# Optimization experiments

Hardware: AMD Instinct MI355X
Metric: run time of the kernel (lower is better)

The kernel has to match this reference:

```python
import jax, jax.numpy as jnp
import numpy as np

N_NODES = 100000
N_EDGES = 1600000
D = 128


def setup_inputs() -> dict:
    key = jax.random.key(0)
    ks = jax.random.split(key, 10)
    s = 1.0 / np.sqrt(D)
    return {
        "feat": jax.random.normal(ks[0], (N_NODES, D), dtype=jnp.float32),
        "W_self0": jax.random.normal(ks[1], (D, D), dtype=jnp.float32) * s,
        "W_neigh0": jax.random.normal(ks[2], (D, D), dtype=jnp.float32) * s,
        "b0": jnp.zeros((D,), dtype=jnp.float32),
        "W_self1": jax.random.normal(ks[3], (D, D), dtype=jnp.float32) * s,
        "W_neigh1": jax.random.normal(ks[4], (D, D), dtype=jnp.float32) * s,
        "b1": jnp.zeros((D,), dtype=jnp.float32),
        "ln_g": jnp.ones((D,), dtype=jnp.float32),
        "ln_b": jnp.zeros((D,), dtype=jnp.float32),
        "edge_src": jax.random.randint(ks[5], (N_EDGES,), 0, N_NODES, dtype=jnp.int32),
        "edge_dst": jax.random.randint(ks[6], (N_EDGES,), 0, N_NODES, dtype=jnp.int32),
        "in_deg": jax.random.randint(ks[7], (N_NODES,), 1, 64, dtype=jnp.int32),
    }


def _sage_layer(h, src, dst, inv_deg, W_self, W_neigh, b):
    # mean aggregation over incoming neighbors: gather -> segment_sum -> scale
    msg = jax.ops.segment_sum(h[src], dst, num_segments=N_NODES)  # [N, d]
    h_neigh = msg * inv_deg[:, None]
    return h @ W_self + h_neigh @ W_neigh + b


def _layer_norm(x, g, b, eps=1e-5):
    mu = jnp.mean(x, axis=-1, keepdims=True)
    var = jnp.mean((x - mu) ** 2, axis=-1, keepdims=True)
    return (x - mu) * jax.lax.rsqrt(var + eps) * g + b


def reference(feat, W_self0, W_neigh0, b0, W_self1, W_neigh1, b1, ln_g, ln_b,
              edge_src, edge_dst, in_deg):
    # Eval mode: dropout = identity, no EmbeddingSelector / reg loss.
    inv_deg = 1.0 / jnp.maximum(in_deg, 1).astype(feat.dtype)
    h = _sage_layer(feat, edge_src, edge_dst, inv_deg, W_self0, W_neigh0, b0)
    h = _layer_norm(h, ln_g, ln_b)
    h = jax.nn.relu(h)
    h = _sage_layer(h, edge_src, edge_dst, inv_deg, W_self1, W_neigh1, b1)
    return h
```

## Files before the change

kernel.cpp:

```cpp
#include <hip/hip_runtime.h>

#define D 128
#define NN 100000
#define PB 391
#define EPB 4096
#define PREP_BLKS 12756

typedef __attribute__((ext_vector_type(8))) short short8;
typedef __attribute__((ext_vector_type(16))) float floatx16;
typedef __attribute__((ext_vector_type(2))) float floatx2;

__device__ inline unsigned short bf16_rne(float f) {
    unsigned int u = __float_as_uint(f);
    u += 0x7fff + ((u >> 16) & 1);
    return (unsigned short)(u >> 16);
}
__device__ inline unsigned char fp8_enc1(float f) {
    return (unsigned char)(__builtin_amdgcn_cvt_pk_fp8_f32(f, f, 0, false) & 0xff);
}


__global__ __launch_bounds__(256) void prep_count_kernel(
    const float* __restrict__ feat, unsigned short* __restrict__ feat16,
    unsigned char* __restrict__ feat8,
    const float* __restrict__ Ws0, const float* __restrict__ Wn0,
    const float* __restrict__ Ws1, const float* __restrict__ Wn1,
    unsigned short* __restrict__ wt0, unsigned short* __restrict__ wt1,
    const int* __restrict__ dst, unsigned int* __restrict__ bucketCnt,
    unsigned int* __restrict__ blockBase, int E)
{
    __shared__ unsigned int h[PB];
    int bid = blockIdx.x;
    if (bid < 12500) {
        int i = bid * 256 + threadIdx.x;
        float4 v = *(const float4*)(feat + (size_t)i * 4);
        unsigned short u[4] = { bf16_rne(v.x), bf16_rne(v.y), bf16_rne(v.z), bf16_rne(v.w) };
        int n  = i >> 5;
        int d0 = (i & 31) * 4;
        size_t f = (size_t)(n >> 5) * 4096 + (size_t)((d0 >> 3) * 32 + (n & 31)) * 8 + (d0 & 7);
        *(uint2*)(feat16 + f) = *(uint2*)u;
        int w = __builtin_amdgcn_cvt_pk_fp8_f32(v.x, v.y, 0, false);
        w = __builtin_amdgcn_cvt_pk_fp8_f32(v.z, v.w, w, true);
        ((unsigned int*)feat8)[i] = (unsigned int)w;
    } else if (bid < PREP_BLKS) {
        int i = (bid - 12500) * 256 + threadIdx.x;
        int layer = i >> 15;
        int r = i & 32767;
        int n = r >> 8;
        int k = r & 255;
        const float* Ws = layer ? Ws1 : Ws0;
        const float* Wn = layer ? Wn1 : Wn0;
        float v = (k < 128) ? Ws[(size_t)k * 128 + n] : Wn[(size_t)(k - 128) * 128 + n];
        unsigned short* wt = layer ? wt1 : wt0;
        int ct = n >> 5, nn = n & 31;
        int hs = k >> 7, k7 = k & 127;
        int kc = k7 >> 4, hf = (k7 >> 3) & 1, j = k7 & 7;
        int frag = ((((ct * 2 + hs) * 8 + kc) * 2 + hf) * 32 + nn) * 8 + j;
        wt[frag] = bf16_rne(v);
    } else {
        const int b = bid - PREP_BLKS;
        const int t = threadIdx.x;
        for (int i = t; i < PB; i += 256) h[i] = 0;
        __syncthreads();
        const int base = b * EPB;
#pragma unroll
        for (int k = 0; k < EPB / 256; k++) {
            int e = base + k * 256 + t;
            if (e < E) atomicAdd(&h[(unsigned)dst[e] >> 8], 1u);
        }
        __syncthreads();
        for (int i = t; i < PB; i += 256) {
            unsigned int c = h[i];
            unsigned int o = 0;
            if (c) o = atomicAdd(&bucketCnt[i], c);
            blockBase[(size_t)b * PB + i] = o;
        }
    }
}

__global__ __launch_bounds__(512) void part_scan_kernel(
    const unsigned int* __restrict__ bucketCnt, unsigned int* __restrict__ bucketStart,
    int E)
{
    __shared__ unsigned int sd[512];
    int t = threadIdx.x;
    unsigned int v = (t < PB) ? bucketCnt[t] : 0u;
    sd[t] = v; __syncthreads();
    for (int off = 1; off < 512; off <<= 1) {
        unsigned int x = (t >= off) ? sd[t - off] : 0u;
        __syncthreads();
        sd[t] += x;
        __syncthreads();
    }
    if (t < PB) bucketStart[t] = sd[t] - v;
    if (t == 0) bucketStart[PB] = (unsigned int)E;
}

__global__ __launch_bounds__(256) void part_scatter_kernel(
    const int* __restrict__ src, const int* __restrict__ dst,
    const unsigned int* __restrict__ bucketStart,
    const unsigned int* __restrict__ blockBase,
    unsigned int* __restrict__ pairs, int E)
{
    __shared__ unsigned int h[PB];
    const int t = threadIdx.x;
    const int b = blockIdx.x;
    for (int i = t; i < PB; i += 256) h[i] = 0;
    __syncthreads();
    const int base = b * EPB;
#pragma unroll
    for (int k = 0; k < EPB / 256; k++) {
        int e = base + k * 256 + t;
        if (e < E) {
            unsigned int d = (unsigned int)dst[e];
            unsigned int bk = d >> 8;
            unsigned int lr = atomicAdd(&h[bk], 1u);
            unsigned int pos = bucketStart[bk] + blockBase[(size_t)b * PB + bk] + lr;
            pairs[pos] = ((unsigned int)src[e] << 8) | (d & 255u);
        }
    }
}

__global__ __launch_bounds__(256) void part_fine_kernel(
    const unsigned int* __restrict__ pairs, const unsigned int* __restrict__ bucketStart,
    int* __restrict__ row_ptr, int* __restrict__ col, int N, int E)
{
    __shared__ unsigned int h[256], sc[256], pos[256];
    const int t = threadIdx.x;
    const int b = blockIdx.x;
    h[t] = 0;
    __syncthreads();
    const unsigned int ebeg = bucketStart[b];
    const unsigned int eend = bucketStart[b + 1];
    for (unsigned int i = ebeg + t; i < eend; i += 256)
        atomicAdd(&h[pairs[i] & 255u], 1u);
    __syncthreads();
    sc[t] = h[t]; __syncthreads();
    for (int off = 1; off < 256; off <<= 1) {
        unsigned int x = (t >= off) ? sc[t - off] : 0u;
        __syncthreads();
        sc[t] += x;
        __syncthreads();
    }
    unsigned int excl = sc[t] - h[t];
    int node = b * 256 + t;
    if (node < N) row_ptr[node] = (int)(ebeg + excl);
    pos[t] = ebeg + excl;
    if (b == 0 && t == 0) row_ptr[N] = E;
    __syncthreads();
    for (unsigned int i = ebeg + t; i < eend; i += 256) {
        unsigned int p = pairs[i];
        unsigned int w = atomicAdd(&pos[p & 255u], 1u);
        col[w] = (int)(p >> 8);
    }
}

__global__ __launch_bounds__(256) void gather8_kernel(
    const unsigned char* __restrict__ h8, const int* __restrict__ row_ptr,
    const int* __restrict__ col, const int* __restrict__ in_deg,
    unsigned short* __restrict__ msg16, int N)
{
    const int wave = threadIdx.x >> 6;
    const int lane = threadIdx.x & 63;
    const int quad = lane >> 4;
    const int ln16 = lane & 15;
    const int node = (blockIdx.x * 4 + wave) * 4 + quad;
    if (node >= N) return;

    const size_t lo = (size_t)ln16 * 8;
    int beg = row_ptr[node];
    int end = row_ptr[node + 1];

    float f[8] = {0.f,0.f,0.f,0.f,0.f,0.f,0.f,0.f};
    int j = beg;
    for (; j + 4 <= end; j += 4) {
        int c0 = col[j], c1 = col[j + 1], c2 = col[j + 2], c3 = col[j + 3];
        uint2 u0 = *(const uint2*)(h8 + (size_t)c0 * D + lo);
        uint2 u1 = *(const uint2*)(h8 + (size_t)c1 * D + lo);
        uint2 u2 = *(const uint2*)(h8 + (size_t)c2 * D + lo);
        uint2 u3 = *(const uint2*)(h8 + (size_t)c3 * D + lo);
#pragma unroll
        for (int q = 0; q < 4; q++) {
            uint2 u = q == 0 ? u0 : q == 1 ? u1 : q == 2 ? u2 : u3;
            floatx2 p0 = __builtin_amdgcn_cvt_pk_f32_fp8((int)u.x, false);
            floatx2 p1 = __builtin_amdgcn_cvt_pk_f32_fp8((int)u.x, true);
            floatx2 p2 = __builtin_amdgcn_cvt_pk_f32_fp8((int)u.y, false);
            floatx2 p3 = __builtin_amdgcn_cvt_pk_f32_fp8((int)u.y, true);
            f[0] += p0.x; f[1] += p0.y; f[2] += p1.x; f[3] += p1.y;
            f[4] += p2.x; f[5] += p2.y; f[6] += p3.x; f[7] += p3.y;
        }
    }
    for (; j < end; ++j) {
        uint2 u = *(const uint2*)(h8 + (size_t)col[j] * D + lo);
        floatx2 p0 = __builtin_amdgcn_cvt_pk_f32_fp8((int)u.x, false);
        floatx2 p1 = __builtin_amdgcn_cvt_pk_f32_fp8((int)u.x, true);
        floatx2 p2 = __builtin_amdgcn_cvt_pk_f32_fp8((int)u.y, false);
        floatx2 p3 = __builtin_amdgcn_cvt_pk_f32_fp8((int)u.y, true);
        f[0] += p0.x; f[1] += p0.y; f[2] += p1.x; f[3] += p1.y;
        f[4] += p2.x; f[5] += p2.y; f[6] += p3.x; f[7] += p3.y;
    }
    int dg = in_deg[node];
    float invd = 1.f / (float)(dg > 1 ? dg : 1);
    unsigned short us[8];
#pragma unroll
    for (int i = 0; i < 8; i++) us[i] = bf16_rne(f[i] * invd);
    size_t fo = (size_t)(node >> 5) * 4096 + ((size_t)ln16 * 32 + (node & 31)) * 8;
    *(uint4*)(msg16 + fo) = *(const uint4*)us;
}

__global__ __launch_bounds__(256, 3) void mfma32_kernel(
    const unsigned short* __restrict__ A16, const unsigned short* __restrict__ Msg16,
    const unsigned short* __restrict__ Wt,
    const float* __restrict__ bias,
    const float* __restrict__ ln_g, const float* __restrict__ ln_b,
    unsigned short* __restrict__ Out16, unsigned char* __restrict__ Out8,
    float* __restrict__ Out32, int N, int do_ln)
{
    __shared__ char smem[49152];

    const int tid  = threadIdx.x;
    const int wave = tid >> 6;
    const int lane = tid & 63;
    const int half = lane >> 5;
    const int n32  = lane & 31;
    const int brow0 = blockIdx.x * 128;
    const int wrow0 = brow0 + wave * 32;

    const int NT = N >> 5;
    int tile = wrow0 >> 5;
    if (tile >= NT) tile = NT - 1;
    const short8* Af = (const short8*)(A16   + (size_t)tile * 4096);
    const short8* Mf = (const short8*)(Msg16 + (size_t)tile * 4096);

    floatx16 acc[4];
#pragma unroll
    for (int ct = 0; ct < 4; ct++)
#pragma unroll
        for (int r = 0; r < 16; r++) acc[ct][r] = 0.f;

#pragma unroll
    for (int hs = 0; hs < 2; hs++) {
        const short8* Sf = hs ? Mf : Af;
#pragma unroll
        for (int kc = 0; kc < 8; kc++) {
            short8 a = Sf[kc * 64 + lane];
#pragma unroll
            for (int ct = 0; ct < 4; ct++) {
                short8 b = *(const short8*)(Wt + ((size_t)((ct * 2 + hs) * 8 + kc) * 64 + lane) * 8);
                acc[ct] = __builtin_amdgcn_mfma_f32_32x32x16_bf16(a, b, acc[ct], 0, 0, 0);
            }
        }
    }

    float bb[4];
#pragma unroll
    for (int ct = 0; ct < 4; ct++) bb[ct] = bias[ct * 32 + n32];

    float v[4][16];
#pragma unroll
    for (int ct = 0; ct < 4; ct++)
#pragma unroll
        for (int r = 0; r < 16; r++) v[ct][r] = acc[ct][r] + bb[ct];

    if (do_ln) {
        float gg[4], be[4];
#pragma unroll
        for (int ct = 0; ct < 4; ct++) {
            gg[ct] = ln_g[ct * 32 + n32];
            be[ct] = ln_b[ct * 32 + n32];
        }
        float s[16], s2[16];
#pragma unroll
        for (int r = 0; r < 16; r++) {
            s[r]  = v[0][r] + v[1][r] + v[2][r] + v[3][r];
            s2[r] = v[0][r]*v[0][r] + v[1][r]*v[1][r] + v[2][r]*v[2][r] + v[3][r]*v[3][r];
        }
#pragma unroll
        for (int off = 1; off < 32; off <<= 1) {
#pragma unroll
            for (int r = 0; r < 16; r++) {
                s[r]  += __shfl_xor(s[r],  off);
                s2[r] += __shfl_xor(s2[r], off);
            }
        }
        unsigned char* sO8 = (unsigned char*)smem + 32768;
#pragma unroll
        for (int r = 0; r < 16; r++) {
            float mean = s[r] * (1.f / 128.f);
            float var  = s2[r] * (1.f / 128.f) - mean * mean;
            float rstd = rsqrtf(var + 1e-5f);
            int brow = wave * 32 + (r & 3) + 8 * (r >> 2) + 4 * half;
#pragma unroll
            for (int ct = 0; ct < 4; ct++) {
                float t = (v[ct][r] - mean) * rstd * gg[ct] + be[ct];
                t = t > 0.f ? t : 0.f;
                int slot = (ct * 4 + (n32 >> 3)) ^ (brow & 15);
                *(unsigned short*)(smem + brow * 256 + slot * 16 + (n32 & 7) * 2) = bf16_rne(t);
                sO8[brow * 128 + ct * 32 + n32] = fp8_enc1(t);
            }
        }
        __syncthreads();
#pragma unroll
        for (int i = 0; i < 8; i++) {
            int ch = tid + i * 256;
            int tl = ch >> 9, p = ch & 511, kc2 = p >> 5, rr = p & 31;
            if (brow0 + tl * 32 + rr < N)
                *(uint4*)(Out16 + (size_t)brow0 * D + ch * 8) =
                    *(const uint4*)&smem[(tl * 32 + rr) * 256 + ((kc2 ^ (rr & 15)) * 16)];
        }
#pragma unroll
        for (int i = 0; i < 4; i++) {
            int ch = tid + i * 256;
            if (brow0 + (ch >> 3) < N)
                *(uint4*)(Out8 + (size_t)brow0 * D + ch * 16) = *(const uint4*)&sO8[ch * 16];
        }
    } else {
#pragma unroll
        for (int r = 0; r < 16; r++) {
            int row = wrow0 + (r & 3) + 8 * (r >> 2) + 4 * half;
            if (row < N) {
#pragma unroll
                for (int ct = 0; ct < 4; ct++)
                    Out32[(size_t)row * D + ct * 32 + n32] = v[ct][r];
            }
        }
    }
}

extern "C" void kernel_launch(void* const* d_in, const int* in_sizes, int n_in,
                              void* d_out, int out_size, void* d_ws, size_t ws_size,
                              hipStream_t stream)
{
    const float* feat = (const float*)d_in[0];
    const float* Ws0  = (const float*)d_in[1];
    const float* Wn0  = (const float*)d_in[2];
    const float* b0   = (const float*)d_in[3];
    const float* Ws1  = (const float*)d_in[4];
    const float* Wn1  = (const float*)d_in[5];
    const float* b1   = (const float*)d_in[6];
    const float* lng  = (const float*)d_in[7];
    const float* lnb  = (const float*)d_in[8];
    const int* esrc   = (const int*)d_in[9];
    const int* edst   = (const int*)d_in[10];
    const int* indeg  = (const int*)d_in[11];

    const int N = NN;
    const int E = in_sizes[9];

    float* out = (float*)d_out;

    const int nblk = (E + EPB - 1) / EPB;
    char* ws = (char*)d_ws;
    size_t o = 0;
    auto alloc = [&](size_t bytes) { char* p = ws + o; o += (bytes + 15) & ~(size_t)15; return p; };
    unsigned short* feat16 = (unsigned short*)alloc((size_t)N * D * 2);
    int* col     = (int*)alloc((size_t)E * 4);
    int* row_ptr = (int*)alloc((size_t)(N + 1) * 4);
    unsigned short* wt0 = (unsigned short*)alloc(128 * 256 * 2);
    unsigned short* wt1 = (unsigned short*)alloc(128 * 256 * 2);
    size_t csr_bytes = (size_t)(512 + 512 + (size_t)nblk * PB + E) * 4 + 64;
    char* regD = alloc((size_t)N * D * 2 > csr_bytes ? (size_t)N * D * 2 : csr_bytes);
    unsigned int* bucketCnt   = (unsigned int*)regD;
    unsigned int* bucketStart = bucketCnt + 512;
    unsigned int* blockBase   = bucketStart + 512;
    unsigned int* pairs       = blockBase + (size_t)nblk * PB;
    unsigned short* h116 = (unsigned short*)regD;

    unsigned short* msg0  = (unsigned short*)d_out;
    unsigned char*  feat8 = (unsigned char*)d_out + (size_t)N * D * 2;
    unsigned char*  h18   = (unsigned char*)d_out + (size_t)N * D * 3;
    unsigned short* msg1  = feat16;
    (void)ws_size;

    const int gemm_blocks = (N + 127) / 128;
    const int gather_blocks = (N + 15) / 16;

    hipMemsetAsync(bucketCnt, 0, 512 * 4, stream);
    prep_count_kernel<<<PREP_BLKS + nblk, 256, 0, stream>>>(
        feat, feat16, feat8, Ws0, Wn0, Ws1, Wn1, wt0, wt1,
        edst, bucketCnt, blockBase, E);

    part_scan_kernel<<<1, 512, 0, stream>>>(bucketCnt, bucketStart, E);
    part_scatter_kernel<<<nblk, 256, 0, stream>>>(esrc, edst, bucketStart, blockBase, pairs, E);
    part_fine_kernel<<<PB, 256, 0, stream>>>(pairs, bucketStart, row_ptr, col, N, E);

    gather8_kernel<<<gather_blocks, 256, 0, stream>>>(feat8, row_ptr, col, indeg, msg0, N);
    mfma32_kernel<<<gemm_blocks, 256, 0, stream>>>(
        feat16, msg0, wt0, b0, lng, lnb, h116, h18, nullptr, N, 1);

    gather8_kernel<<<gather_blocks, 256, 0, stream>>>(h18, row_ptr, col, indeg, msg1, N);
    mfma32_kernel<<<gemm_blocks, 256, 0, stream>>>(
        h116, msg1, wt1, b1, nullptr, nullptr, nullptr, nullptr, out, N, 0);
}
```

Before: 308.8 us.

## Fuse layer-0 neighbor gather into GEMM+LayerNorm kernel via shared memory

Layer 0 now uses a single kernel. Each 128-row block first gathers and mean-aggregates the fp8 neighbor features into a swizzled LDS tile, then runs the MFMA GEMM and LayerNorm/ReLU epilogue, so the bf16 message buffer is never written to or read back from global memory. Layer 1 keeps a separate gather, now staged through LDS so its global stores are coalesced, and the GEMM kernel is reduced to the non-LN path. The trade-off is that the gather phase now shares occupancy and LDS with the GEMM phase, and each block works through 8 serial gather rounds, which may hurt latency hiding for the random gathers.

```diff
diff --git a/kernel.cpp b/kernel.cpp
--- a/kernel.cpp
+++ b/kernel.cpp
@@ -155,69 +155,247 @@
     }
 }
 
-__global__ __launch_bounds__(256) void gather8_kernel(
+__global__ __launch_bounds__(256, 3) void sage_layer_kernel(
+    const unsigned short* __restrict__ A16,
+    const unsigned char*  __restrict__ H8,
+    const int* __restrict__ row_ptr, const int* __restrict__ col,
+    const int* __restrict__ in_deg,
+    const unsigned short* __restrict__ Wt,
+    const float* __restrict__ bias,
+    const float* __restrict__ ln_g, const float* __restrict__ ln_b,
+    unsigned short* __restrict__ Out16, unsigned char* __restrict__ Out8,
+    int N)
+{
+    __shared__ char smem[49152];
+
+    const int tid  = threadIdx.x;
+    const int wave = tid >> 6;
+    const int lane = tid & 63;
+    const int half = lane >> 5;
+    const int n32  = lane & 31;
+    const int quad = lane >> 4;
+    const int ln16 = lane & 15;
+    const int nq   = wave * 4 + quad;
+    const int brow0 = blockIdx.x * 128;
+
+    {
+        const size_t lo = (size_t)ln16 * 8;
+#pragma unroll 1
+        for (int rep = 0; rep < 8; rep++) {
+            int lr = rep * 16 + nq;
+            int node = brow0 + lr;
+            if (node < N) {
+                int beg = row_ptr[node];
+                int end = row_ptr[node + 1];
+                float f[8] = {0.f,0.f,0.f,0.f,0.f,0.f,0.f,0.f};
+                int j = beg;
+                for (; j + 4 <= end; j += 4) {
+                    int c0 = col[j], c1 = col[j + 1], c2 = col[j + 2], c3 = col[j + 3];
+                    uint2 u0 = *(const uint2*)(H8 + (size_t)c0 * D + lo);
+                    uint2 u1 = *(const uint2*)(H8 + (size_t)c1 * D + lo);
+                    uint2 u2 = *(const uint2*)(H8 + (size_t)c2 * D + lo);
+                    uint2 u3 = *(const uint2*)(H8 + (size_t)c3 * D + lo);
+#pragma unroll
+                    for (int q = 0; q < 4; q++) {
+                        uint2 u = q == 0 ? u0 : q == 1 ? u1 : q == 2 ? u2 : u3;
+                        floatx2 p0 = __builtin_amdgcn_cvt_pk_f32_fp8((int)u.x, false);
+                        floatx2 p1 = __builtin_amdgcn_cvt_pk_f32_fp8((int)u.x, true);
+                        floatx2 p2 = __builtin_amdgcn_cvt_pk_f32_fp8((int)u.y, false);
+                        floatx2 p3 = __builtin_amdgcn_cvt_pk_f32_fp8((int)u.y, true);
+                        f[0] += p0.x; f[1] += p0.y; f[2] += p1.x; f[3] += p1.y;
+                        f[4] += p2.x; f[5] += p2.y; f[6] += p3.x; f[7] += p3.y;
+                    }
+                }
+                for (; j < end; ++j) {
+                    uint2 u = *(const uint2*)(H8 + (size_t)col[j] * D + lo);
+                    floatx2 p0 = __builtin_amdgcn_cvt_pk_f32_fp8((int)u.x, false);
+                    floatx2 p1 = __builtin_amdgcn_cvt_pk_f32_fp8((int)u.x, true);
+                    floatx2 p2 = __builtin_amdgcn_cvt_pk_f32_fp8((int)u.y, false);
+                    floatx2 p3 = __builtin_amdgcn_cvt_pk_f32_fp8((int)u.y, true);
+                    f[0] += p0.x; f[1] += p0.y; f[2] += p1.x; f[3] += p1.y;
+                    f[4] += p2.x; f[5] += p2.y; f[6] += p3.x; f[7] += p3.y;
+                }
+                int dg = in_deg[node];
+                float invd = 1.f / (float)(dg > 1 ? dg : 1);
+                unsigned short us[8];
+#pragma unroll
+                for (int i = 0; i < 8; i++) us[i] = bf16_rne(f[i] * invd);
+                int ci = ((lr >> 5) << 9) + (ln16 << 5) + (lr & 31);
+                int sl = ci ^ ((ci >> 5) & 7);
+                *(uint4*)(smem + sl * 16) = *(const uint4*)us;
+            }
+        }
+    }
+    __syncthreads();
+
+    const int NT = N >> 5;
+    int tile = (brow0 >> 5) + wave;
+    if (tile >= NT) tile = NT - 1;
+    const short8* Af = (const short8*)(A16 + (size_t)tile * 4096);
+
+    floatx16 acc[4];
+#pragma unroll
+    for (int ct = 0; ct < 4; ct++)
+#pragma unroll
+        for (int r = 0; r < 16; r++) acc[ct][r] = 0.f;
+
+#pragma unroll
+    for (int kc = 0; kc < 8; kc++) {
+        short8 a = Af[kc * 64 + lane];
+#pragma unroll
+        for (int ct = 0; ct < 4; ct++) {
+            short8 b = *(const short8*)(Wt + ((size_t)((ct * 2 + 0) * 8 + kc) * 64 + lane) * 8);
+            acc[ct] = __builtin_amdgcn_mfma_f32_32x32x16_bf16(a, b, acc[ct], 0, 0, 0);
+        }
+    }
+#pragma unroll
+    for (int kc = 0; kc < 8; kc++) {
+        int ci = (wave << 9) + (kc << 6) + lane;
+        int sl = ci ^ ((ci >> 5) & 7);
+        short8 a = *(const short8*)(smem + sl * 16);
+#pragma unroll
+        for (int ct = 0; ct < 4; ct++) {
+            short8 b = *(const short8*)(Wt + ((size_t)((ct * 2 + 1) * 8 + kc) * 64 + lane) * 8);
+            acc[ct] = __builtin_amdgcn_mfma_f32_32x32x16_bf16(a, b, acc[ct], 0, 0, 0);
+        }
+    }
+
+    float bb[4], gg[4], be[4];
+#pragma unroll
+    for (int ct = 0; ct < 4; ct++) {
+        bb[ct] = bias[ct * 32 + n32];
+        gg[ct] = ln_g[ct * 32 + n32];
+        be[ct] = ln_b[ct * 32 + n32];
+    }
+    float v[4][16];
+#pragma unroll
+    for (int ct = 0; ct < 4; ct++)
+#pragma unroll
+        for (int r = 0; r < 16; r++) v[ct][r] = acc[ct][r] + bb[ct];
+
+    float s[16], s2[16];
+#pragma unroll
+    for (int r = 0; r < 16; r++) {
+        s[r]  = v[0][r] + v[1][r] + v[2][r] + v[3][r];
+        s2[r] = v[0][r]*v[0][r] + v[1][r]*v[1][r] + v[2][r]*v[2][r] + v[3][r]*v[3][r];
+    }
+#pragma unroll
+    for (int off = 1; off < 32; off <<= 1) {
+#pragma unroll
+        for (int r = 0; r < 16; r++) {
+            s[r]  += __shfl_xor(s[r],  off);
+            s2[r] += __shfl_xor(s2[r], off);
+        }
+    }
+    __syncthreads();
+    unsigned char* sO8 = (unsigned char*)smem + 32768;
+#pragma unroll
+    for (int r = 0; r < 16; r++) {
+        float mean = s[r] * (1.f / 128.f);
+        float var  = s2[r] * (1.f / 128.f) - mean * mean;
+        float rstd = rsqrtf(var + 1e-5f);
+        int brow = wave * 32 + (r & 3) + 8 * (r >> 2) + 4 * half;
+#pragma unroll
+        for (int ct = 0; ct < 4; ct++) {
+            float t = (v[ct][r] - mean) * rstd * gg[ct] + be[ct];
+            t = t > 0.f ? t : 0.f;
+            int slot = (ct * 4 + (n32 >> 3)) ^ (brow & 15);
+            *(unsigned short*)(smem + brow * 256 + slot * 16 + (n32 & 7) * 2) = bf16_rne(t);
+            sO8[brow * 128 + ct * 32 + n32] = fp8_enc1(t);
+        }
+    }
+    __syncthreads();
+#pragma unroll
+    for (int i = 0; i < 8; i++) {
+        int ch = tid + i * 256;
+        int tl = ch >> 9, p = ch & 511, kc2 = p >> 5, rr = p & 31;
+        if (brow0 + tl * 32 + rr < N)
+            *(uint4*)(Out16 + (size_t)brow0 * D + ch * 8) =
+                *(const uint4*)&smem[(tl * 32 + rr) * 256 + ((kc2 ^ (rr & 15)) * 16)];
+    }
+#pragma unroll
+    for (int i = 0; i < 4; i++) {
+        int ch = tid + i * 256;
+        if (brow0 + (ch >> 3) < N)
+            *(uint4*)(Out8 + (size_t)brow0 * D + ch * 16) = *(const uint4*)&sO8[ch * 16];
+    }
+}
+
+__global__ __launch_bounds__(256) void gather8f_kernel(
     const unsigned char* __restrict__ h8, const int* __restrict__ row_ptr,
     const int* __restrict__ col, const int* __restrict__ in_deg,
     unsigned short* __restrict__ msg16, int N)
 {
-    const int wave = threadIdx.x >> 6;
-    const int lane = threadIdx.x & 63;
-    const int quad = lane >> 4;
-    const int ln16 = lane & 15;
-    const int node = (blockIdx.x * 4 + wave) * 4 + quad;
-    if (node >= N) return;
-
+    __shared__ char smem[32768];
+    const int tid  = threadIdx.x;
+    const int nq   = tid >> 4;
+    const int ln16 = tid & 15;
+    const int brow0 = blockIdx.x * 128;
     const size_t lo = (size_t)ln16 * 8;
-    int beg = row_ptr[node];
-    int end = row_ptr[node + 1];
-
-    float f[8] = {0.f,0.f,0.f,0.f,0.f,0.f,0.f,0.f};
-    int j = beg;
-    for (; j + 4 <= end; j += 4) {
-        int c0 = col[j], c1 = col[j + 1], c2 = col[j + 2], c3 = col[j + 3];
-        uint2 u0 = *(const uint2*)(h8 + (size_t)c0 * D + lo);
-        uint2 u1 = *(const uint2*)(h8 + (size_t)c1 * D + lo);
-        uint2 u2 = *(const uint2*)(h8 + (size_t)c2 * D + lo);
-        uint2 u3 = *(const uint2*)(h8 + (size_t)c3 * D + lo);
-#pragma unroll
-        for (int q = 0; q < 4; q++) {
-            uint2 u = q == 0 ? u0 : q == 1 ? u1 : q == 2 ? u2 : u3;
-            floatx2 p0 = __builtin_amdgcn_cvt_pk_f32_fp8((int)u.x, false);
-            floatx2 p1 = __builtin_amdgcn_cvt_pk_f32_fp8((int)u.x, true);
-            floatx2 p2 = __builtin_amdgcn_cvt_pk_f32_fp8((int)u.y, false);
-            floatx2 p3 = __builtin_amdgcn_cvt_pk_f32_fp8((int)u.y, true);
-            f[0] += p0.x; f[1] += p0.y; f[2] += p1.x; f[3] += p1.y;
-            f[4] += p2.x; f[5] += p2.y; f[6] += p3.x; f[7] += p3.y;
-        }
-    }
-    for (; j < end; ++j) {
-        uint2 u = *(const uint2*)(h8 + (size_t)col[j] * D + lo);
-        floatx2 p0 = __builtin_amdgcn_cvt_pk_f32_fp8((int)u.x, false);
-        floatx2 p1 = __builtin_amdgcn_cvt_pk_f32_fp8((int)u.x, true);
-        floatx2 p2 = __builtin_amdgcn_cvt_pk_f32_fp8((int)u.y, false);
-        floatx2 p3 = __builtin_amdgcn_cvt_pk_f32_fp8((int)u.y, true);
-        f[0] += p0.x; f[1] += p0.y; f[2] += p1.x; f[3] += p1.y;
-        f[4] += p2.x; f[5] += p2.y; f[6] += p3.x; f[7] += p3.y;
-    }
-    int dg = in_deg[node];
-    float invd = 1.f / (float)(dg > 1 ? dg : 1);
-    unsigned short us[8];
-#pragma unroll
-    for (int i = 0; i < 8; i++) us[i] = bf16_rne(f[i] * invd);
-    size_t fo = (size_t)(node >> 5) * 4096 + ((size_t)ln16 * 32 + (node & 31)) * 8;
-    *(uint4*)(msg16 + fo) = *(const uint4*)us;
+
+#pragma unroll 1
+    for (int rep = 0; rep < 8; rep++) {
+        int lr = rep * 16 + nq;
+        int node = brow0 + lr;
+        if (node < N) {
+            int beg = row_ptr[node];
+            int end = row_ptr[node + 1];
+            float f[8] = {0.f,0.f,0.f,0.f,0.f,0.f,0.f,0.f};
+            int j = beg;
+            for (; j + 4 <= end; j += 4) {
+                int c0 = col[j], c1 = col[j + 1], c2 = col[j + 2], c3 = col[j + 3];
+                uint2 u0 = *(const uint2*)(h8 + (size_t)c0 * D + lo);
+                uint2 u1 = *(const uint2*)(h8 + (size_t)c1 * D + lo);
+                uint2 u2 = *(const uint2*)(h8 + (size_t)c2 * D + lo);
+                uint2 u3 = *(const uint2*)(h8 + (size_t)c3 * D + lo);
+#pragma unroll
+                for (int q = 0; q < 4; q++) {
+                    uint2 u = q == 0 ? u0 : q == 1 ? u1 : q == 2 ? u2 : u3;
+                    floatx2 p0 = __builtin_amdgcn_cvt_pk_f32_fp8((int)u.x, false);
+                    floatx2 p1 = __builtin_amdgcn_cvt_pk_f32_fp8((int)u.x, true);
+                    floatx2 p2 = __builtin_amdgcn_cvt_pk_f32_fp8((int)u.y, false);
+                    floatx2 p3 = __builtin_amdgcn_cvt_pk_f32_fp8((int)u.y, true);
+                    f[0] += p0.x; f[1] += p0.y; f[2] += p1.x; f[3] += p1.y;
+                    f[4] += p2.x; f[5] += p2.y; f[6] += p3.x; f[7] += p3.y;
+                }
+            }
+            for (; j < end; ++j) {
+                uint2 u = *(const uint2*)(h8 + (size_t)col[j] * D + lo);
+                floatx2 p0 = __builtin_amdgcn_cvt_pk_f32_fp8((int)u.x, false);
+                floatx2 p1 = __builtin_amdgcn_cvt_pk_f32_fp8((int)u.x, true);
+                floatx2 p2 = __builtin_amdgcn_cvt_pk_f32_fp8((int)u.y, false);
+                floatx2 p3 = __builtin_amdgcn_cvt_pk_f32_fp8((int)u.y, true);
+                f[0] += p0.x; f[1] += p0.y; f[2] += p1.x; f[3] += p1.y;
+                f[4] += p2.x; f[5] += p2.y; f[6] += p3.x; f[7] += p3.y;
+            }
+            int dg = in_deg[node];
+            float invd = 1.f / (float)(dg > 1 ? dg : 1);
+            unsigned short us[8];
+#pragma unroll
+            for (int i = 0; i < 8; i++) us[i] = bf16_rne(f[i] * invd);
+            int ci = ((lr >> 5) << 9) + (ln16 << 5) + (lr & 31);
+            int sl = ci ^ ((ci >> 5) & 7);
+            *(uint4*)(smem + sl * 16) = *(const uint4*)us;
+        }
+    }
+    __syncthreads();
+#pragma unroll
+    for (int i = 0; i < 8; i++) {
+        int ch = tid + i * 256;
+        int row = brow0 + ((ch >> 9) << 5) + (ch & 31);
+        if (row < N) {
+            int sl = ch ^ ((ch >> 5) & 7);
+            *(uint4*)(msg16 + (size_t)brow0 * D + ch * 8) = *(const uint4*)(smem + sl * 16);
+        }
+    }
 }
 
 __global__ __launch_bounds__(256, 3) void mfma32_kernel(
     const unsigned short* __restrict__ A16, const unsigned short* __restrict__ Msg16,
     const unsigned short* __restrict__ Wt,
     const float* __restrict__ bias,
-    const float* __restrict__ ln_g, const float* __restrict__ ln_b,
-    unsigned short* __restrict__ Out16, unsigned char* __restrict__ Out8,
-    float* __restrict__ Out32, int N, int do_ln)
-{
-    __shared__ char smem[49152];
-
+    float* __restrict__ Out32, int N)
+{
     const int tid  = threadIdx.x;
     const int wave = tid >> 6;
     const int lane = tid & 63;
@@ -256,73 +434,13 @@
 #pragma unroll
     for (int ct = 0; ct < 4; ct++) bb[ct] = bias[ct * 32 + n32];
 
-    float v[4][16];
-#pragma unroll
-    for (int ct = 0; ct < 4; ct++)
-#pragma unroll
-        for (int r = 0; r < 16; r++) v[ct][r] = acc[ct][r] + bb[ct];
-
-    if (do_ln) {
-        float gg[4], be[4];
-#pragma unroll
-        for (int ct = 0; ct < 4; ct++) {
-            gg[ct] = ln_g[ct * 32 + n32];
-            be[ct] = ln_b[ct * 32 + n32];
-        }
-        float s[16], s2[16];
-#pragma unroll
-        for (int r = 0; r < 16; r++) {
-            s[r]  = v[0][r] + v[1][r] + v[2][r] + v[3][r];
-            s2[r] = v[0][r]*v[0][r] + v[1][r]*v[1][r] + v[2][r]*v[2][r] + v[3][r]*v[3][r];
-        }
-#pragma unroll
-        for (int off = 1; off < 32; off <<= 1) {
-#pragma unroll
-            for (int r = 0; r < 16; r++) {
-                s[r]  += __shfl_xor(s[r],  off);
-                s2[r] += __shfl_xor(s2[r], off);
-            }
-        }
-        unsigned char* sO8 = (unsigned char*)smem + 32768;
-#pragma unroll
-        for (int r = 0; r < 16; r++) {
-            float mean = s[r] * (1.f / 128.f);
-            float var  = s2[r] * (1.f / 128.f) - mean * mean;
-            float rstd = rsqrtf(var + 1e-5f);
-            int brow = wave * 32 + (r & 3) + 8 * (r >> 2) + 4 * half;
-#pragma unroll
-            for (int ct = 0; ct < 4; ct++) {
-                float t = (v[ct][r] - mean) * rstd * gg[ct] + be[ct];
-                t = t > 0.f ? t : 0.f;
-                int slot = (ct * 4 + (n32 >> 3)) ^ (brow & 15);
-                *(unsigned short*)(smem + brow * 256 + slot * 16 + (n32 & 7) * 2) = bf16_rne(t);
-                sO8[brow * 128 + ct * 32 + n32] = fp8_enc1(t);
-            }
-        }
-        __syncthreads();
-#pragma unroll
-        for (int i = 0; i < 8; i++) {
-            int ch = tid + i * 256;
-            int tl = ch >> 9, p = ch & 511, kc2 = p >> 5, rr = p & 31;
-            if (brow0 + tl * 32 + rr < N)
-                *(uint4*)(Out16 + (size_t)brow0 * D + ch * 8) =
-                    *(const uint4*)&smem[(tl * 32 + rr) * 256 + ((kc2 ^ (rr & 15)) * 16)];
-        }
-#pragma unroll
-        for (int i = 0; i < 4; i++) {
-            int ch = tid + i * 256;
-            if (brow0 + (ch >> 3) < N)
-                *(uint4*)(Out8 + (size_t)brow0 * D + ch * 16) = *(const uint4*)&sO8[ch * 16];
-        }
-    } else {
-#pragma unroll
-        for (int r = 0; r < 16; r++) {
-            int row = wrow0 + (r & 3) + 8 * (r >> 2) + 4 * half;
-            if (row < N) {
-#pragma unroll
-                for (int ct = 0; ct < 4; ct++)
-                    Out32[(size_t)row * D + ct * 32 + n32] = v[ct][r];
-            }
+#pragma unroll
+    for (int r = 0; r < 16; r++) {
+        int row = wrow0 + (r & 3) + 8 * (r >> 2) + 4 * half;
+        if (row < N) {
+#pragma unroll
+            for (int ct = 0; ct < 4; ct++)
+                Out32[(size_t)row * D + ct * 32 + n32] = acc[ct][r] + bb[ct];
         }
     }
 }
@@ -366,14 +484,12 @@
     unsigned int* pairs       = blockBase + (size_t)nblk * PB;
     unsigned short* h116 = (unsigned short*)regD;
 
-    unsigned short* msg0  = (unsigned short*)d_out;
     unsigned char*  feat8 = (unsigned char*)d_out + (size_t)N * D * 2;
     unsigned char*  h18   = (unsigned char*)d_out + (size_t)N * D * 3;
-    unsigned short* msg1  = feat16;
+    unsigned short* msg1F = feat16;
     (void)ws_size;
 
     const int gemm_blocks = (N + 127) / 128;
-    const int gather_blocks = (N + 15) / 16;
 
     hipMemsetAsync(bucketCnt, 0, 512 * 4, stream);
     prep_count_kernel<<<PREP_BLKS + nblk, 256, 0, stream>>>(
@@ -384,11 +500,10 @@
     part_scatter_kernel<<<nblk, 256, 0, stream>>>(esrc, edst, bucketStart, blockBase, pairs, E);
     part_fine_kernel<<<PB, 256, 0, stream>>>(pairs, bucketStart, row_ptr, col, N, E);
 
-    gather8_kernel<<<gather_blocks, 256, 0, stream>>>(feat8, row_ptr, col, indeg, msg0, N);
-    mfma32_kernel<<<gemm_blocks, 256, 0, stream>>>(
-        feat16, msg0, wt0, b0, lng, lnb, h116, h18, nullptr, N, 1);
-
-    gather8_kernel<<<gather_blocks, 256, 0, stream>>>(h18, row_ptr, col, indeg, msg1, N);
-    mfma32_kernel<<<gemm_blocks, 256, 0, stream>>>(
-        h116, msg1, wt1, b1, nullptr, nullptr, nullptr, nullptr, out, N, 0);
-}
+    sage_layer_kernel<<<gemm_blocks, 256, 0, stream>>>(
+        feat16, feat8, row_ptr, col, indeg, wt0, b0, lng, lnb,
+        h116, h18, N);
+
+    gather8f_kernel<<<gemm_blocks, 256, 0, stream>>>(h18, row_ptr, col, indeg, msg1F, N);
+    mfma32_kernel<<<gemm_blocks, 256, 0, stream>>>(h116, msg1F, wt1, b1, out, N);
+}
```

Result: slower. 379.2 us (+22.8%).
